# Optimization experiments

Hardware: AMD Instinct MI355X
Metric: run time of the kernel (lower is better)

## Reference

```python
import jax, jax.numpy as jnp
import numpy as np

def setup_inputs() -> dict:
    key = jax.random.key(0)
    k1, k2, k3 = jax.random.split(key, 3)
    B, K = 32, 64
    n1, n2, n3 = 4, 8, 8
    b1, b2, b3 = 256, 4, 4
    y = jax.random.normal(k1, (B, K, n1, n2, n3), dtype=jnp.float32)
    W1d = jax.random.normal(k2, (K, 1, b1, 1, 1), dtype=jnp.float32)
    W2d = jax.random.normal(k3, (K, 1, 1, b2, b3), dtype=jnp.float32)
    return {"y": y, "W1d": W1d, "W2d": W2d}

def reference(y, W1d, W2d):
    # y: (B, K, n1, n2, n3); W1d: (K,1,b1,1,1); W2d: (K,1,1,b2,b3)
    B, K, n1, n2, n3 = y.shape
    b1 = W1d.shape[2]
    b2, b3 = W2d.shape[3], W2d.shape[4]
    w1 = W1d[:, 0, :, 0, 0]      # (K, b1)
    w2 = W2d[:, 0, 0, :, :]      # (K, b2, b3)
    # xhat[b, d1*b1+i, d2*b2+j, d3*b3+l] = sum_k y[b,k,d1,d2,d3]*w1[k,i]*w2[k,j,l]
    blocks = jnp.einsum('bkxyz,ki,kjl->bxiyjzl', y, w1, w2)  # (B,n1,b1,n2,b2,n3,b3)
    xhat = blocks.reshape(B, 1, n1 * b1, n2 * b2, n3 * b3)
    return xhat
```

## Files before the change

### kernel.cpp

```cpp
#include <hip/hip_runtime.h>


typedef __bf16 bf16x8 __attribute__((ext_vector_type(8)));
typedef float  f32x4  __attribute__((ext_vector_type(4)));

#define LDK 72

__device__ __forceinline__ unsigned short f2bf(float f) {
    union { float f; unsigned u; } v; v.f = f;
    unsigned r = v.u + 0x7fffu + ((v.u >> 16) & 1u);
    return (unsigned short)(r >> 16);
}
__device__ __forceinline__ unsigned pack2(float a, float b) {
    return (unsigned)f2bf(a) | ((unsigned)f2bf(b) << 16);
}

__global__ __launch_bounds__(256)
void backproj_kernel(const float* __restrict__ y,
                     const float* __restrict__ w1,
                     const float* __restrict__ w2,
                     float* __restrict__ out)
{
    __shared__ float y_s[64 * 8];
    __shared__ __align__(16) unsigned short sT[128 * LDK];

    const int bid = blockIdx.x;
    const int iq  = bid & 3;
    const int yy  = (bid >> 2) & 7;
    const int x   = (bid >> 5) & 3;
    const int b   = bid >> 7;

    const int tid  = threadIdx.x;
    const int wave = tid >> 6, lane = tid & 63;
    const int la   = lane & 15, quad = lane >> 4;

    if (tid < 128) {
        const float* ybase = y + (size_t)b * 16384 + x * 64 + yy * 8;
        int k = tid >> 1, h = tid & 1;
        ((float4*)y_s)[tid] = ((const float4*)(ybase + k * 256))[h];
    }

    bf16x8 a0, a1;
    {
        const float* wcol = w1 + iq * 64 + wave * 16 + la;
        union { unsigned u[4]; bf16x8 v; } ua, ub;
        #pragma unroll
        for (int j = 0; j < 8; j += 2) {
            float f0 = wcol[(quad * 8 + j) * 256];
            float f1 = wcol[(quad * 8 + j + 1) * 256];
            float g0 = wcol[(32 + quad * 8 + j) * 256];
            float g1 = wcol[(32 + quad * 8 + j + 1) * 256];
            ua.u[j >> 1] = pack2(f0, f1);
            ub.u[j >> 1] = pack2(g0, g1);
        }
        a0 = ua.v; a1 = ub.v;
    }

    __syncthreads();

    {
        const int c  = tid >> 1;
        const int kh = (tid & 1) * 32;
        const int j = c >> 5, z = (c >> 2) & 7, l = c & 3;
        const float* w2p = w2 + j * 4 + l;
        unsigned* dst = (unsigned*)&sT[c * LDK + kh];
        #pragma unroll
        for (int kk = 0; kk < 32; kk += 2) {
            float f0 = y_s[(kh + kk) * 8 + z]     * w2p[(kh + kk) * 16];
            float f1 = y_s[(kh + kk + 1) * 8 + z] * w2p[(kh + kk + 1) * 16];
            dst[kk >> 1] = pack2(f0, f1);
        }
    }
    __syncthreads();

    f32x4 acc[8];
    #pragma unroll
    for (int mt = 0; mt < 8; ++mt) acc[mt] = (f32x4){0.f, 0.f, 0.f, 0.f};

    #pragma unroll
    for (int mt = 0; mt < 8; ++mt) {
        const bf16x8 b0 = *(const bf16x8*)&sT[(mt * 16 + la) * LDK + quad * 8];
        const bf16x8 b1 = *(const bf16x8*)&sT[(mt * 16 + la) * LDK + 32 + quad * 8];
        acc[mt] = __builtin_amdgcn_mfma_f32_16x16x32_bf16(a0, b0, acc[mt], 0, 0, 0);
        acc[mt] = __builtin_amdgcn_mfma_f32_16x16x32_bf16(a1, b1, acc[mt], 0, 0, 0);
    }

    const int i_row0 = iq * 64 + wave * 16 + quad * 4;
    float* op = out + ((size_t)(b * 1024 + x * 256 + i_row0)) * 1024 + yy * 128 + la;
    #pragma unroll
    for (int mt = 0; mt < 8; ++mt) {
        float* o = op + mt * 16;
        o[0]    = acc[mt][0];
        o[1024] = acc[mt][1];
        o[2048] = acc[mt][2];
        o[3072] = acc[mt][3];
    }
}

extern "C" void kernel_launch(void* const* d_in, const int* in_sizes, int n_in,
                              void* d_out, int out_size, void* d_ws, size_t ws_size,
                              hipStream_t stream) {
    const float* y  = (const float*)d_in[0];
    const float* w1 = (const float*)d_in[1];
    const float* w2 = (const float*)d_in[2];
    float* out = (float*)d_out;

    backproj_kernel<<<dim3(4096), dim3(256), 0, stream>>>(y, w1, w2, out);
}
```

Before: 152.4 us.

## Merge four i-quarter blocks into one 512-thread block with shared B tile

Each block now covers all 256 rows of i for a given (b,x,yy) using 8 waves with two 16-row tiles each, instead of four separate blocks each rebuilding the same y*w2 B tile. It also stages y and w2 transposed in LDS so the B-tile build uses vector LDS reads rather than scattered global w2 loads. The aim is to cut redundant B-tile construction and global loads, in exchange for fewer, larger blocks and more accumulator registers per thread.

```diff
diff --git a/kernel.cpp b/kernel.cpp
--- a/kernel.cpp
+++ b/kernel.cpp
@@ -5,6 +5,7 @@
 typedef float  f32x4  __attribute__((ext_vector_type(4)));
 
 #define LDK 72
+#define YLD 68
 
 __device__ __forceinline__ unsigned short f2bf(float f) {
     union { float f; unsigned u; } v; v.f = f;
@@ -15,85 +16,114 @@
     return (unsigned)f2bf(a) | ((unsigned)f2bf(b) << 16);
 }
 
-__global__ __launch_bounds__(256)
+__global__ __launch_bounds__(512, 4)
 void backproj_kernel(const float* __restrict__ y,
                      const float* __restrict__ w1,
                      const float* __restrict__ w2,
                      float* __restrict__ out)
 {
-    __shared__ float y_s[64 * 8];
+    __shared__ float y_sT[8 * YLD];
+    __shared__ float w2T[16 * YLD];
     __shared__ __align__(16) unsigned short sT[128 * LDK];
 
     const int bid = blockIdx.x;
-    const int iq  = bid & 3;
-    const int yy  = (bid >> 2) & 7;
-    const int x   = (bid >> 5) & 3;
-    const int b   = bid >> 7;
+    const int yy = bid & 7;
+    const int x  = (bid >> 3) & 3;
+    const int b  = bid >> 5;
 
     const int tid  = threadIdx.x;
-    const int wave = tid >> 6, lane = tid & 63;
+    const int wv   = tid >> 6, lane = tid & 63;
     const int la   = lane & 15, quad = lane >> 4;
 
+    float4 yv = {0.f, 0.f, 0.f, 0.f}, wvv = {0.f, 0.f, 0.f, 0.f};
     if (tid < 128) {
-        const float* ybase = y + (size_t)b * 16384 + x * 64 + yy * 8;
+        const float* ybase = y + b * 16384 + x * 64 + yy * 8;
         int k = tid >> 1, h = tid & 1;
-        ((float4*)y_s)[tid] = ((const float4*)(ybase + k * 256))[h];
+        yv = ((const float4*)(ybase + k * 256))[h];
+    } else if (tid < 384) {
+        int idx = tid - 128;
+        int k = idx >> 2, g = idx & 3;
+        wvv = ((const float4*)(w2 + k * 16))[g];
     }
 
-    bf16x8 a0, a1;
-    {
-        const float* wcol = w1 + iq * 64 + wave * 16 + la;
-        union { unsigned u[4]; bf16x8 v; } ua, ub;
+    bf16x8 a[2][2];
+    #pragma unroll
+    for (int it = 0; it < 2; ++it) {
+        const float* wcol = w1 + wv * 32 + it * 16 + la;
+        union { unsigned u[4]; bf16x8 v; } u0, u1;
         #pragma unroll
-        for (int j = 0; j < 8; j += 2) {
-            float f0 = wcol[(quad * 8 + j) * 256];
-            float f1 = wcol[(quad * 8 + j + 1) * 256];
-            float g0 = wcol[(32 + quad * 8 + j) * 256];
-            float g1 = wcol[(32 + quad * 8 + j + 1) * 256];
-            ua.u[j >> 1] = pack2(f0, f1);
-            ub.u[j >> 1] = pack2(g0, g1);
+        for (int j2 = 0; j2 < 4; ++j2) {
+            float f0 = wcol[(quad * 8 + 2 * j2) * 256];
+            float f1 = wcol[(quad * 8 + 2 * j2 + 1) * 256];
+            float g0 = wcol[(32 + quad * 8 + 2 * j2) * 256];
+            float g1 = wcol[(32 + quad * 8 + 2 * j2 + 1) * 256];
+            u0.u[j2] = pack2(f0, f1);
+            u1.u[j2] = pack2(g0, g1);
         }
-        a0 = ua.v; a1 = ub.v;
+        a[it][0] = u0.v; a[it][1] = u1.v;
     }
 
+    if (tid < 128) {
+        int k = tid >> 1, h = tid & 1;
+        y_sT[(h * 4 + 0) * YLD + k] = yv.x;
+        y_sT[(h * 4 + 1) * YLD + k] = yv.y;
+        y_sT[(h * 4 + 2) * YLD + k] = yv.z;
+        y_sT[(h * 4 + 3) * YLD + k] = yv.w;
+    } else if (tid < 384) {
+        int idx = tid - 128;
+        int k = idx >> 2, g = idx & 3;
+        w2T[(g * 4 + 0) * YLD + k] = wvv.x;
+        w2T[(g * 4 + 1) * YLD + k] = wvv.y;
+        w2T[(g * 4 + 2) * YLD + k] = wvv.z;
+        w2T[(g * 4 + 3) * YLD + k] = wvv.w;
+    }
     __syncthreads();
 
     {
-        const int c  = tid >> 1;
-        const int kh = (tid & 1) * 32;
-        const int j = c >> 5, z = (c >> 2) & 7, l = c & 3;
-        const float* w2p = w2 + j * 4 + l;
-        unsigned* dst = (unsigned*)&sT[c * LDK + kh];
+        const int c  = tid >> 2;
+        const int kq = (tid & 3) * 16;
+        const int z  = (c >> 2) & 7;
+        const int jl = (c >> 5) * 4 + (c & 3);
+        const f32x4* yp = (const f32x4*)&y_sT[z * YLD + kq];
+        const f32x4* wp = (const f32x4*)&w2T[jl * YLD + kq];
+        unsigned* dst = (unsigned*)&sT[c * LDK + kq];
         #pragma unroll
-        for (int kk = 0; kk < 32; kk += 2) {
-            float f0 = y_s[(kh + kk) * 8 + z]     * w2p[(kh + kk) * 16];
-            float f1 = y_s[(kh + kk + 1) * 8 + z] * w2p[(kh + kk + 1) * 16];
-            dst[kk >> 1] = pack2(f0, f1);
+        for (int q = 0; q < 4; ++q) {
+            f32x4 a4 = yp[q], b4 = wp[q];
+            dst[q * 2 + 0] = pack2(a4[0] * b4[0], a4[1] * b4[1]);
+            dst[q * 2 + 1] = pack2(a4[2] * b4[2], a4[3] * b4[3]);
         }
     }
     __syncthreads();
 
-    f32x4 acc[8];
+    f32x4 acc[2][8];
     #pragma unroll
-    for (int mt = 0; mt < 8; ++mt) acc[mt] = (f32x4){0.f, 0.f, 0.f, 0.f};
+    for (int it = 0; it < 2; ++it)
+        #pragma unroll
+        for (int mt = 0; mt < 8; ++mt) acc[it][mt] = (f32x4){0.f, 0.f, 0.f, 0.f};
 
     #pragma unroll
     for (int mt = 0; mt < 8; ++mt) {
         const bf16x8 b0 = *(const bf16x8*)&sT[(mt * 16 + la) * LDK + quad * 8];
         const bf16x8 b1 = *(const bf16x8*)&sT[(mt * 16 + la) * LDK + 32 + quad * 8];
-        acc[mt] = __builtin_amdgcn_mfma_f32_16x16x32_bf16(a0, b0, acc[mt], 0, 0, 0);
-        acc[mt] = __builtin_amdgcn_mfma_f32_16x16x32_bf16(a1, b1, acc[mt], 0, 0, 0);
+        acc[0][mt] = __builtin_amdgcn_mfma_f32_16x16x32_bf16(a[0][0], b0, acc[0][mt], 0, 0, 0);
+        acc[0][mt] = __builtin_amdgcn_mfma_f32_16x16x32_bf16(a[0][1], b1, acc[0][mt], 0, 0, 0);
+        acc[1][mt] = __builtin_amdgcn_mfma_f32_16x16x32_bf16(a[1][0], b0, acc[1][mt], 0, 0, 0);
+        acc[1][mt] = __builtin_amdgcn_mfma_f32_16x16x32_bf16(a[1][1], b1, acc[1][mt], 0, 0, 0);
     }
 
-    const int i_row0 = iq * 64 + wave * 16 + quad * 4;
-    float* op = out + ((size_t)(b * 1024 + x * 256 + i_row0)) * 1024 + yy * 128 + la;
     #pragma unroll
-    for (int mt = 0; mt < 8; ++mt) {
-        float* o = op + mt * 16;
-        o[0]    = acc[mt][0];
-        o[1024] = acc[mt][1];
-        o[2048] = acc[mt][2];
-        o[3072] = acc[mt][3];
+    for (int it = 0; it < 2; ++it) {
+        const int i0 = wv * 32 + it * 16 + quad * 4;
+        float* op = out + (size_t)(b * 1024 + x * 256 + i0) * 1024 + yy * 128 + la;
+        #pragma unroll
+        for (int mt = 0; mt < 8; ++mt) {
+            float* o = op + mt * 16;
+            o[0]    = acc[it][mt][0];
+            o[1024] = acc[it][mt][1];
+            o[2048] = acc[it][mt][2];
+            o[3072] = acc[it][mt][3];
+        }
     }
 }
 
@@ -105,5 +135,5 @@
     const float* w2 = (const float*)d_in[2];
     float* out = (float*)d_out;
 
-    backproj_kernel<<<dim3(4096), dim3(256), 0, stream>>>(y, w1, w2, out);
+    backproj_kernel<<<dim3(1024), dim3(512), 0, stream>>>(y, w1, w2, out);
 }
```

After: 139.7 us. 8.3% less time.

## Enlarge blocks to cover full output rows and pretranspose w1 to bf16

Applied to the files above, without the earlier changes.

Each block now covers a (b, x, half-of-i) tile with 512 threads, building the full 1024-column y*w2 operand in shared memory once and sweeping all 64 column tiles. Operands are swapped in the MFMA so each lane writes contiguous float4 rows of output. A small prep kernel writes w1 transposed to bf16 in the workspace so the A fragments become vector loads instead of strided gathers. The aim is to cut redundant w1/y loads and operand rebuilds across blocks and to widen stores, at the cost of fewer blocks (256) with large shared memory (about 147KB) and one extra launch.

```diff
diff --git a/kernel.cpp b/kernel.cpp
--- a/kernel.cpp
+++ b/kernel.cpp
@@ -4,7 +4,8 @@
 typedef __bf16 bf16x8 __attribute__((ext_vector_type(8)));
 typedef float  f32x4  __attribute__((ext_vector_type(4)));
 
-#define LDK 72
+#define LDK  72
+#define W2LD 68
 
 __device__ __forceinline__ unsigned short f2bf(float f) {
     union { float f; unsigned u; } v; v.f = f;
@@ -16,84 +17,97 @@
 }
 
 __global__ __launch_bounds__(256)
+void prep_w1(const float* __restrict__ w1, unsigned short* __restrict__ w1T) {
+    int t = blockIdx.x * 256 + threadIdx.x;
+    int i = t >> 6, k = t & 63;
+    w1T[t] = f2bf(w1[k * 256 + i]);
+}
+
+template <bool PRE>
+__global__ __launch_bounds__(512, 1)
 void backproj_kernel(const float* __restrict__ y,
                      const float* __restrict__ w1,
+                     const unsigned short* __restrict__ w1T,
                      const float* __restrict__ w2,
                      float* __restrict__ out)
 {
-    __shared__ float y_s[64 * 8];
-    __shared__ __align__(16) unsigned short sT[128 * LDK];
+    __shared__ __align__(16) unsigned short sTall[1024 * LDK];
+    __shared__ float w2T[16 * W2LD];
 
     const int bid = blockIdx.x;
-    const int iq  = bid & 3;
-    const int yy  = (bid >> 2) & 7;
-    const int x   = (bid >> 5) & 3;
-    const int b   = bid >> 7;
+    const int ih = bid & 1;
+    const int x  = (bid >> 1) & 3;
+    const int b  = bid >> 3;
 
     const int tid  = threadIdx.x;
-    const int wave = tid >> 6, lane = tid & 63;
+    const int wv   = tid >> 6, lane = tid & 63;
     const int la   = lane & 15, quad = lane >> 4;
+    const int i0   = ih * 128 + wv * 16;
 
-    if (tid < 128) {
-        const float* ybase = y + (size_t)b * 16384 + x * 64 + yy * 8;
-        int k = tid >> 1, h = tid & 1;
-        ((float4*)y_s)[tid] = ((const float4*)(ybase + k * 256))[h];
+    if (tid < 256) {
+        int k = tid >> 2, g = tid & 3;
+        float4 wvv = ((const float4*)(w2 + k * 16))[g];
+        w2T[(g * 4 + 0) * W2LD + k] = wvv.x;
+        w2T[(g * 4 + 1) * W2LD + k] = wvv.y;
+        w2T[(g * 4 + 2) * W2LD + k] = wvv.z;
+        w2T[(g * 4 + 3) * W2LD + k] = wvv.w;
     }
 
     bf16x8 a0, a1;
-    {
-        const float* wcol = w1 + iq * 64 + wave * 16 + la;
-        union { unsigned u[4]; bf16x8 v; } ua, ub;
+    if (PRE) {
+        const unsigned short* p = w1T + (i0 + la) * 64 + quad * 8;
+        a0 = *(const bf16x8*)p;
+        a1 = *(const bf16x8*)(p + 32);
+    } else {
+        const float* wcol = w1 + i0 + la;
+        union { unsigned u[4]; bf16x8 v; } u0, u1;
         #pragma unroll
-        for (int j = 0; j < 8; j += 2) {
-            float f0 = wcol[(quad * 8 + j) * 256];
-            float f1 = wcol[(quad * 8 + j + 1) * 256];
-            float g0 = wcol[(32 + quad * 8 + j) * 256];
-            float g1 = wcol[(32 + quad * 8 + j + 1) * 256];
-            ua.u[j >> 1] = pack2(f0, f1);
-            ub.u[j >> 1] = pack2(g0, g1);
+        for (int j2 = 0; j2 < 4; ++j2) {
+            float f0 = wcol[(quad * 8 + 2 * j2) * 256];
+            float f1 = wcol[(quad * 8 + 2 * j2 + 1) * 256];
+            float g0 = wcol[(32 + quad * 8 + 2 * j2) * 256];
+            float g1 = wcol[(32 + quad * 8 + 2 * j2 + 1) * 256];
+            u0.u[j2] = pack2(f0, f1);
+            u1.u[j2] = pack2(g0, g1);
         }
-        a0 = ua.v; a1 = ub.v;
+        a0 = u0.v; a1 = u1.v;
     }
 
     __syncthreads();
 
     {
-        const int c  = tid >> 1;
-        const int kh = (tid & 1) * 32;
-        const int j = c >> 5, z = (c >> 2) & 7, l = c & 3;
-        const float* w2p = w2 + j * 4 + l;
-        unsigned* dst = (unsigned*)&sT[c * LDK + kh];
+        const int c0  = tid, c1 = tid + 512;
+        const int yy0 = c0 >> 7, yy1 = yy0 + 4;
+        const int j   = (c0 >> 5) & 3, z = (c0 >> 2) & 7, l = c0 & 3;
+        const int jl  = j * 4 + l;
+        const float* yg0 = y + b * 16384 + x * 64 + yy0 * 8 + z;
+        const float* yg1 = y + b * 16384 + x * 64 + yy1 * 8 + z;
+        unsigned* d0 = (unsigned*)&sTall[c0 * LDK];
+        unsigned* d1 = (unsigned*)&sTall[c1 * LDK];
         #pragma unroll
-        for (int kk = 0; kk < 32; kk += 2) {
-            float f0 = y_s[(kh + kk) * 8 + z]     * w2p[(kh + kk) * 16];
-            float f1 = y_s[(kh + kk + 1) * 8 + z] * w2p[(kh + kk + 1) * 16];
-            dst[kk >> 1] = pack2(f0, f1);
+        for (int q = 0; q < 16; ++q) {
+            f32x4 wq = *(const f32x4*)&w2T[jl * W2LD + q * 4];
+            float p0 = yg0[(q * 4 + 0) * 256], p1 = yg0[(q * 4 + 1) * 256];
+            float p2 = yg0[(q * 4 + 2) * 256], p3 = yg0[(q * 4 + 3) * 256];
+            float r0 = yg1[(q * 4 + 0) * 256], r1 = yg1[(q * 4 + 1) * 256];
+            float r2 = yg1[(q * 4 + 2) * 256], r3 = yg1[(q * 4 + 3) * 256];
+            d0[2 * q]     = pack2(p0 * wq[0], p1 * wq[1]);
+            d0[2 * q + 1] = pack2(p2 * wq[2], p3 * wq[3]);
+            d1[2 * q]     = pack2(r0 * wq[0], r1 * wq[1]);
+            d1[2 * q + 1] = pack2(r2 * wq[2], r3 * wq[3]);
         }
     }
     __syncthreads();
 
-    f32x4 acc[8];
-    #pragma unroll
-    for (int mt = 0; mt < 8; ++mt) acc[mt] = (f32x4){0.f, 0.f, 0.f, 0.f};
-
-    #pragma unroll
-    for (int mt = 0; mt < 8; ++mt) {
-        const bf16x8 b0 = *(const bf16x8*)&sT[(mt * 16 + la) * LDK + quad * 8];
-        const bf16x8 b1 = *(const bf16x8*)&sT[(mt * 16 + la) * LDK + 32 + quad * 8];
-        acc[mt] = __builtin_amdgcn_mfma_f32_16x16x32_bf16(a0, b0, acc[mt], 0, 0, 0);
-        acc[mt] = __builtin_amdgcn_mfma_f32_16x16x32_bf16(a1, b1, acc[mt], 0, 0, 0);
-    }
-
-    const int i_row0 = iq * 64 + wave * 16 + quad * 4;
-    float* op = out + ((size_t)(b * 1024 + x * 256 + i_row0)) * 1024 + yy * 128 + la;
-    #pragma unroll
-    for (int mt = 0; mt < 8; ++mt) {
-        float* o = op + mt * 16;
-        o[0]    = acc[mt][0];
-        o[1024] = acc[mt][1];
-        o[2048] = acc[mt][2];
-        o[3072] = acc[mt][3];
+    float* rowp = out + (size_t)(b * 1024 + x * 256 + i0 + la) * 1024 + quad * 4;
+    #pragma unroll 4
+    for (int ct = 0; ct < 64; ++ct) {
+        const bf16x8 b0 = *(const bf16x8*)&sTall[(ct * 16 + la) * LDK + quad * 8];
+        const bf16x8 b1 = *(const bf16x8*)&sTall[(ct * 16 + la) * LDK + 32 + quad * 8];
+        f32x4 acc = (f32x4){0.f, 0.f, 0.f, 0.f};
+        acc = __builtin_amdgcn_mfma_f32_16x16x32_bf16(b0, a0, acc, 0, 0, 0);
+        acc = __builtin_amdgcn_mfma_f32_16x16x32_bf16(b1, a1, acc, 0, 0, 0);
+        *(f32x4*)(rowp + ct * 16) = acc;
     }
 }
 
@@ -105,5 +119,11 @@
     const float* w2 = (const float*)d_in[2];
     float* out = (float*)d_out;
 
-    backproj_kernel<<<dim3(4096), dim3(256), 0, stream>>>(y, w1, w2, out);
+    if (ws_size >= 32768 && d_ws != nullptr) {
+        unsigned short* w1T = (unsigned short*)d_ws;
+        prep_w1<<<dim3(64), dim3(256), 0, stream>>>(w1, w1T);
+        backproj_kernel<true><<<dim3(256), dim3(512), 0, stream>>>(y, w1, w1T, w2, out);
+    } else {
+        backproj_kernel<false><<<dim3(256), dim3(512), 0, stream>>>(y, w1, nullptr, w2, out);
+    }
 }
```

Result: faster. 147.7 us (-3.1%).
